# Kernel optimization log

Measured on AMD Instinct MI355X. Metric: run time of the kernel, lower is better.

## Reference

```python
import jax, jax.numpy as jnp
import numpy as np

OUT = 7            # output_size
SR = 2             # sampling_ratio (samples per bin per axis)
SCALES = (0.25, 0.125, 0.0625, 0.03125)
CANON_SIZE = 224.0
CANON_LVL = 4.0
MIN_LVL = 2
IMG = 800.0


def setup_inputs() -> dict:
    key = jax.random.key(0)
    kf = jax.random.split(key, 6)
    B, C, R = 2, 256, 256
    sizes = [200, 100, 50, 25]
    feats = [jax.random.normal(kf[i], (B, C, s, s), jnp.float32) for i, s in enumerate(sizes)]
    # valid xyxy boxes in [0, IMG], log-uniform side lengths -> spread across FPN levels
    ctr = jax.random.uniform(kf[4], (B, R, 2), minval=0.0, maxval=IMG)
    wh = jnp.exp(jax.random.uniform(kf[5], (B, R, 2), minval=float(np.log(16.0)), maxval=float(np.log(512.0))))
    lo = jnp.clip(ctr - wh / 2, 0.0, IMG)
    hi = jnp.clip(ctr + wh / 2, 0.0, IMG)
    boxes = jnp.concatenate([lo, hi], axis=-1)  # [B,R,4]
    return {"feat0": feats[0], "feat1": feats[1], "feat2": feats[2], "feat3": feats[3], "boxes": boxes}


def _prep(c, lim):
    """torchvision ROIAlign (aligned=False) bilinear index prep.
    c: sample coords [N,OUT,SR]; lim: per-box feature extent (H or W) [N]."""
    limb = lim[:, None, None]
    valid = (c > -1.0) & (c < limb)          # out-of-range samples contribute 0
    cc = jnp.maximum(c, 0.0)
    low = jnp.floor(cc)
    cap = limb - 1.0
    at_edge = low >= cap                      # y_low >= H-1 -> clamp, frac = 0
    low = jnp.minimum(low, cap)
    high = jnp.minimum(low + 1.0, cap)
    cc = jnp.where(at_edge, low, cc)
    frac = cc - low
    return valid, low.astype(jnp.int32), high.astype(jnp.int32), frac


def roi_pooler(feats, boxes):
    B, R = boxes.shape[0], boxes.shape[1]
    C = feats[0].shape[1]
    N = B * R
    flat = boxes.reshape(N, 4)
    bidx = jnp.repeat(jnp.arange(B, dtype=jnp.int32), R)  # batch index per ROI

    # level assignment (assign_boxes_to_levels)
    area = (flat[:, 2] - flat[:, 0]) * (flat[:, 3] - flat[:, 1])
    lvl = jnp.floor(CANON_LVL + jnp.log2(jnp.sqrt(area) / CANON_SIZE + 1e-8))
    lvl = jnp.clip(lvl, MIN_LVL, MIN_LVL + len(feats) - 1).astype(jnp.int32) - MIN_LVL  # [N] in [0,3]

    # pad all levels to P2 size and stack so each ROI is sampled once at its level
    Hm, Wm = feats[0].shape[2], feats[0].shape[3]
    padded = jnp.stack([jnp.pad(f, ((0, 0), (0, 0), (0, Hm - f.shape[2]), (0, Wm - f.shape[3]))) for f in feats])
    fp = padded.transpose(0, 1, 3, 4, 2)  # [L,B,Hm,Wm,C] channels-last for gather
    Hs = jnp.array([f.shape[2] for f in feats], jnp.float32)[lvl]
    Ws = jnp.array([f.shape[3] for f in feats], jnp.float32)[lvl]
    scale = jnp.array(SCALES, jnp.float32)[lvl]

    # ROIAlign aligned=False: scale coords, clamp roi size to >= 1
    x1 = flat[:, 0] * scale
    y1 = flat[:, 1] * scale
    x2 = flat[:, 2] * scale
    y2 = flat[:, 3] * scale
    roi_w = jnp.maximum(x2 - x1, 1.0)
    roi_h = jnp.maximum(y2 - y1, 1.0)
    bw = roi_w / OUT
    bh = roi_h / OUT

    # sample grid: bin index + sub-sample offsets -> [N,OUT,SR]
    grid = jnp.arange(OUT, dtype=jnp.float32)[None, :, None] + (jnp.arange(SR, dtype=jnp.float32)[None, None, :] + 0.5) / SR
    ys = y1[:, None, None] + bh[:, None, None] * grid
    xs = x1[:, None, None] + bw[:, None, None] * grid

    vy, yl, yh, fy = _prep(ys, Hs)
    vx, xl, xh, fx = _prep(xs, Ws)

    P = OUT * OUT * SR * SR  # all sample points per ROI

    def by(a):  # y-axis quantity -> broadcast over (out_y,out_x,sr_y,sr_x)
        return jnp.broadcast_to(a[:, :, None, :, None], (N, OUT, OUT, SR, SR)).reshape(N, P)

    def bx(a):
        return jnp.broadcast_to(a[:, None, :, None, :], (N, OUT, OUT, SR, SR)).reshape(N, P)

    YL, YH, FY, VY = by(yl), by(yh), by(fy), by(vy)
    XL, XH, FX, VX = bx(xl), bx(xh), bx(fx), bx(vx)

    li = lvl[:, None]
    bi = bidx[:, None]
    v00 = fp[li, bi, YL, XL]  # [N,P,C]
    v01 = fp[li, bi, YL, XH]
    v10 = fp[li, bi, YH, XL]
    v11 = fp[li, bi, YH, XH]

    w = lambda a: a[..., None]
    val = (w((1 - FY) * (1 - FX)) * v00 + w((1 - FY) * FX) * v01
           + w(FY * (1 - FX)) * v10 + w(FY * FX) * v11)
    val = val * w((VY & VX).astype(val.dtype))
    out = val.reshape(N, OUT, OUT, SR * SR, C).mean(axis=3)  # average over SR*SR samples
    return out.transpose(0, 3, 1, 2)  # [N,C,OUT,OUT]


def reference(feat0, feat1, feat2, feat3, boxes):
    return roi_pooler([feat0, feat1, feat2, feat3], boxes)
```

## Files before the change

kernel.cpp:

```cpp
#include <hip/hip_runtime.h>
#include <math.h>

typedef unsigned short u16;
typedef unsigned int   u32;

#define OUTSZ 7
#define B_ 2
#define C_ 256
#define R_ 256
#define N_ (B_ * R_)

#define PX_TOTAL 106250
#define WS_NEEDED ((size_t)PX_TOTAL * 256 * 2)

__device__ __forceinline__ u16 f2bf(float v) {
    u32 u = __float_as_uint(v);
    u += 0x7fffu + ((u >> 16) & 1u);
    return (u16)(u >> 16);
}

__device__ __forceinline__ u32 pack2bf(float a, float b) {
    return (u32)f2bf(a) | ((u32)f2bf(b) << 16);
}

__device__ __forceinline__ float bflo(u32 u) { return __uint_as_float(u << 16); }
__device__ __forceinline__ float bfhi(u32 u) { return __uint_as_float(u & 0xffff0000u); }

__global__ __launch_bounds__(512, 8) void nhwc_cast(
    const float* __restrict__ f0, const float* __restrict__ f1,
    const float* __restrict__ f2, const float* __restrict__ f3,
    u16* __restrict__ dst)
{
    __shared__ u32 lds32[256 * 32];
    const int tid  = threadIdx.x;
    const int lane = tid & 63;
    const int wave = tid >> 6;

    const int t  = blockIdx.x;
    const int cb = blockIdx.y;
    const int b  = blockIdx.z;
    const float* src; int HWsz, dstBase, ft;
    if      (t < 157) { src = f0; HWsz = 40000; dstBase = 0;      ft = t;       }
    else if (t < 197) { src = f1; HWsz = 10000; dstBase = 80000;  ft = t - 157; }
    else if (t < 207) { src = f2; HWsz = 2500;  dstBase = 100000; ft = t - 197; }
    else              { src = f3; HWsz = 625;   dstBase = 105000; ft = t - 207; }

    const int fbase = ft * 256;
    const int cw    = cb * 64 + wave * 8;
    const int rem   = HWsz - fbase;
    const int p0    = 4 * lane;
    const bool vec  = ((HWsz & 3) == 0) && (p0 + 3 < rem);

    const float* base = src + ((size_t)(b * C_ + cw)) * HWsz + fbase;

    float f[8][4];
    #pragma unroll
    for (int i = 0; i < 8; ++i) {
        const float* row = base + (size_t)i * HWsz;
        if (vec) {
            float4 v = *(const float4*)(row + p0);
            f[i][0] = v.x; f[i][1] = v.y; f[i][2] = v.z; f[i][3] = v.w;
        } else {
            #pragma unroll
            for (int k = 0; k < 4; ++k)
                f[i][k] = (p0 + k < rem) ? row[p0 + k] : 0.0f;
        }
    }

    #pragma unroll
    for (int j = 0; j < 4; ++j) {
        uint4 o;
        o.x = pack2bf(f[0][j], f[1][j]);
        o.y = pack2bf(f[2][j], f[3][j]);
        o.z = pack2bf(f[4][j], f[5][j]);
        o.w = pack2bf(f[6][j], f[7][j]);
        const int q = wave ^ (lane & 7);
        *(uint4*)&lds32[(p0 + j) * 32 + q * 4] = o;
    }
    __syncthreads();

    const int maxpx = rem < 256 ? rem : 256;
    #pragma unroll
    for (int i = 0; i < 4; ++i) {
        const int idx = i * 512 + tid;
        const int px  = idx >> 3;
        const int sub = idx & 7;
        if (px < maxpx) {
            const int q = sub ^ ((px >> 2) & 7);
            uint4 o = *(const uint4*)&lds32[px * 32 + q * 4];
            *(uint4*)(dst + (size_t)(dstBase + b * HWsz + fbase + px) * 256 + cb * 64 + sub * 8) = o;
        }
    }
}

__global__ __launch_bounds__(512) void roi_gather(
    const u16* __restrict__ ws16, const float* __restrict__ boxes,
    float* __restrict__ out)
{
    __shared__ float ldsO[49 * 264];
    __shared__ float s_wy0[14], s_wy1[14], s_wlo[14], s_whi[14];
    __shared__ int   s_yl[14], s_yh[14], s_xo[14];
    __shared__ int   s_base, s_W;

    const int n    = blockIdx.x;
    const int tid  = threadIdx.x;
    const int lane = tid & 63;
    const int wave = tid >> 6;

    if (tid < 28) {
        const float* bx = boxes + (size_t)n * 4;
        float x1 = bx[0], y1 = bx[1], x2 = bx[2], y2 = bx[3];
        float area = (x2 - x1) * (y2 - y1);
        float lf = floorf(4.0f + log2f(sqrtf(area) / 224.0f + 1e-8f));
        lf = fminf(fmaxf(lf, 2.0f), 5.0f);
        int lvl = (int)lf - 2;
        const float scales[4] = {0.25f, 0.125f, 0.0625f, 0.03125f};
        const int   sizes[4]  = {200, 100, 50, 25};
        const int   bases[4]  = {0, 80000, 100000, 105000};
        float scale = scales[lvl];
        int   HW    = sizes[lvl];
        float lim = (float)HW, cap = lim - 1.0f;
        float fx1 = x1 * scale, fy1 = y1 * scale;
        float bw = fmaxf(x2 * scale - fx1, 1.0f) / (float)OUTSZ;
        float bh = fmaxf(y2 * scale - fy1, 1.0f) / (float)OUTSZ;
        if (tid == 0) { s_base = bases[lvl] + (n >> 8) * HW * HW; s_W = HW; }

        const int  i   = (tid < 14) ? tid : tid - 14;
        const bool isy = tid < 14;
        float o  = isy ? fy1 : fx1;
        float st = isy ? bh  : bw;
        float gq = (float)(i >> 1) + ((float)(i & 1) + 0.5f) * 0.5f;
        float c = o + st * gq;
        bool  v = (c > -1.0f) && (c < lim);
        float cc = fmaxf(c, 0.0f);
        float low = floorf(cc);
        bool  edge = low >= cap;
        low = fminf(low, cap);
        float high = fminf(low + 1.0f, cap);
        float fr = edge ? 0.0f : (cc - low);
        float w0 = v ? (1.0f - fr) : 0.0f;
        float w1 = v ? fr : 0.0f;
        if (isy) {
            s_yl[i] = (int)low; s_yh[i] = (int)high; s_wy0[i] = w0; s_wy1[i] = w1;
        } else {
            int xl = (int)low, xh = (int)high;
            bool col = (xh == xl);
            s_xo[i]  = col ? xl - 1 : xl;
            s_wlo[i] = col ? 0.0f : w0;
            s_whi[i] = col ? (w0 + w1) : w1;
        }
    }
    __syncthreads();

    const int base = s_base, W = s_W;
    const bool hiHalf = lane >= 32;

    for (int cell = wave; cell < 49; cell += 8) {
        const int cu = __builtin_amdgcn_readfirstlane(cell);
        const int oy = cu / 7, ox = cu - oy * 7;
        float a0 = 0, a1 = 0, a2 = 0, a3 = 0, a4 = 0, a5 = 0, a6 = 0, a7 = 0;
        #pragma unroll
        for (int sy = 0; sy < 2; ++sy) {
            const int ei = oy * 2 + sy;
            const float wy0 = s_wy0[ei], wy1 = s_wy1[ei];
            const size_t rl = (size_t)(base + s_yl[ei] * W);
            const size_t rh = (size_t)(base + s_yh[ei] * W);
            #pragma unroll
            for (int sx = 0; sx < 2; ++sx) {
                const int ej = ox * 2 + sx;
                const int xo = s_xo[ej];
                const float wsel = hiHalf ? s_whi[ej] : s_wlo[ej];
                uint4 A = ((const uint4*)(ws16 + (rl + xo) * 256))[lane];
                const float wa = wy0 * wsel;
                a0 += wa * bflo(A.x); a1 += wa * bfhi(A.x);
                a2 += wa * bflo(A.y); a3 += wa * bfhi(A.y);
                a4 += wa * bflo(A.z); a5 += wa * bfhi(A.z);
                a6 += wa * bflo(A.w); a7 += wa * bfhi(A.w);
                uint4 Bv = ((const uint4*)(ws16 + (rh + xo) * 256))[lane];
                const float wb = wy1 * wsel;
                a0 += wb * bflo(Bv.x); a1 += wb * bfhi(Bv.x);
                a2 += wb * bflo(Bv.y); a3 += wb * bfhi(Bv.y);
                a4 += wb * bflo(Bv.z); a5 += wb * bfhi(Bv.z);
                a6 += wb * bflo(Bv.w); a7 += wb * bfhi(Bv.w);
            }
        }
        a0 += __shfl_xor(a0, 32); a1 += __shfl_xor(a1, 32);
        a2 += __shfl_xor(a2, 32); a3 += __shfl_xor(a3, 32);
        a4 += __shfl_xor(a4, 32); a5 += __shfl_xor(a5, 32);
        a6 += __shfl_xor(a6, 32); a7 += __shfl_xor(a7, 32);
        float* dstl = &ldsO[cu * 264 + (lane & 31) * 8 + (hiHalf ? 4 : 0)];
        float4 v = hiHalf ? make_float4(a4 * 0.25f, a5 * 0.25f, a6 * 0.25f, a7 * 0.25f)
                          : make_float4(a0 * 0.25f, a1 * 0.25f, a2 * 0.25f, a3 * 0.25f);
        *(float4*)dstl = v;
    }
    __syncthreads();

    float* op = out + (size_t)n * (C_ * 49);
    for (int i4 = tid; i4 < 3136; i4 += 512) {
        const int e = 4 * i4;
        float4 v;
        {   int c = e / 49,      r = e - 49 * c;          v.x = ldsO[r * 264 + c]; }
        {   int c = (e+1) / 49,  r = (e+1) - 49 * c;      v.y = ldsO[r * 264 + c]; }
        {   int c = (e+2) / 49,  r = (e+2) - 49 * c;      v.z = ldsO[r * 264 + c]; }
        {   int c = (e+3) / 49,  r = (e+3) - 49 * c;      v.w = ldsO[r * 264 + c]; }
        *(float4*)(op + e) = v;
    }
}

__global__ __launch_bounds__(256) void roi_direct(
    const float* __restrict__ f0, const float* __restrict__ f1,
    const float* __restrict__ f2, const float* __restrict__ f3,
    const float* __restrict__ boxes, float* __restrict__ out)
{
    const int total = B_ * R_ * C_ * OUTSZ * OUTSZ;
    int idx = blockIdx.x * blockDim.x + threadIdx.x;
    if (idx >= total) return;
    int ox = idx % 7, oy = (idx / 7) % 7, c = (idx / 49) % C_, n = idx / (49 * C_), b = n >> 8;
    const float* bx = boxes + (size_t)n * 4;
    float x1 = bx[0], y1 = bx[1], x2 = bx[2], y2 = bx[3];
    float lf = floorf(4.0f + log2f(sqrtf((x2 - x1) * (y2 - y1)) / 224.0f + 1e-8f));
    int lvl = (int)fminf(fmaxf(lf, 2.0f), 5.0f) - 2;
    const float scales[4] = {0.25f, 0.125f, 0.0625f, 0.03125f};
    const int sizes[4] = {200, 100, 50, 25};
    float scale = scales[lvl]; int HW = sizes[lvl];
    const float* fl = lvl == 0 ? f0 : lvl == 1 ? f1 : lvl == 2 ? f2 : f3;
    float fx1 = x1 * scale, fy1 = y1 * scale;
    float bw = fmaxf(x2 * scale - fx1, 1.0f) / 7.0f, bh = fmaxf(y2 * scale - fy1, 1.0f) / 7.0f;
    const float* plane = fl + ((size_t)(b * C_ + c)) * HW * HW;
    float lim = (float)HW, cap = lim - 1.0f, acc = 0.0f;
    #pragma unroll
    for (int sy = 0; sy < 2; sy++) {
        float yc = fy1 + bh * ((float)oy + ((float)sy + 0.5f) * 0.5f);
        bool vy = (yc > -1.0f) && (yc < lim);
        float ccy = fmaxf(yc, 0.0f), lowy = floorf(ccy);
        bool ey = lowy >= cap; lowy = fminf(lowy, cap);
        float highy = fminf(lowy + 1.0f, cap);
        float wfy = ey ? 0.0f : (ccy - lowy);
        int yl = (int)lowy, yh = (int)highy;
        #pragma unroll
        for (int sx = 0; sx < 2; sx++) {
            float xc = fx1 + bw * ((float)ox + ((float)sx + 0.5f) * 0.5f);
            bool vx = (xc > -1.0f) && (xc < lim);
            float ccx = fmaxf(xc, 0.0f), lowx = floorf(ccx);
            bool ex = lowx >= cap; lowx = fminf(lowx, cap);
            float highx = fminf(lowx + 1.0f, cap);
            float wfx = ex ? 0.0f : (ccx - lowx);
            int xl = (int)lowx, xh = (int)highx;
            if (vy && vx) {
                float v00 = plane[yl * HW + xl], v01 = plane[yl * HW + xh];
                float v10 = plane[yh * HW + xl], v11 = plane[yh * HW + xh];
                acc += (1.0f - wfy) * ((1.0f - wfx) * v00 + wfx * v01)
                     + wfy * ((1.0f - wfx) * v10 + wfx * v11);
            }
        }
    }
    out[idx] = acc * 0.25f;
}

extern "C" void kernel_launch(void* const* d_in, const int* in_sizes, int n_in,
                              void* d_out, int out_size, void* d_ws, size_t ws_size,
                              hipStream_t stream) {
    const float* f0    = (const float*)d_in[0];
    const float* f1    = (const float*)d_in[1];
    const float* f2    = (const float*)d_in[2];
    const float* f3    = (const float*)d_in[3];
    const float* boxes = (const float*)d_in[4];
    float* out = (float*)d_out;

    if (ws_size < WS_NEEDED) {
        const int total = B_ * R_ * C_ * OUTSZ * OUTSZ;
        roi_direct<<<(total + 255) / 256, 256, 0, stream>>>(f0, f1, f2, f3, boxes, out);
        return;
    }

    u16* nhwc = (u16*)d_ws;

    nhwc_cast<<<dim3(210, 4, 2), 512, 0, stream>>>(f0, f1, f2, f3, nhwc);
    roi_gather<<<dim3(N_), 512, 0, stream>>>(nhwc, boxes, out);
}
```

Before: 180.5 us.

## Split ROI gather across two channel-half blocks with two x-columns per wave

The gather kernel now launches two blocks per ROI, each handling 128 channels, which halves the per-block LDS staging buffer and doubles the block count. Within a wave, the two 32-lane halves now load adjacent x-columns (xo and xo+1) for 128 channels each, using 8-byte loads instead of 16-byte loads. A launch bound of 8 blocks per CU is added to raise occupancy. The cost is that each ROI's box and weight preparation is duplicated across both blocks, the loads are narrower, and only the lower half-wave writes results to LDS.

```diff
diff --git a/kernel.cpp b/kernel.cpp
--- a/kernel.cpp
+++ b/kernel.cpp
@@ -93,16 +93,17 @@
     }
 }
 
-__global__ __launch_bounds__(512) void roi_gather(
+__global__ __launch_bounds__(512, 8) void roi_gather(
     const u16* __restrict__ ws16, const float* __restrict__ boxes,
     float* __restrict__ out)
 {
-    __shared__ float ldsO[49 * 264];
+    __shared__ float ldsO[49 * 132];
     __shared__ float s_wy0[14], s_wy1[14], s_wlo[14], s_whi[14];
     __shared__ int   s_yl[14], s_yh[14], s_xo[14];
     __shared__ int   s_base, s_W;
 
-    const int n    = blockIdx.x;
+    const int g    = blockIdx.x;
+    const int n    = blockIdx.y;
     const int tid  = threadIdx.x;
     const int lane = tid & 63;
     const int wave = tid >> 6;
@@ -153,12 +154,15 @@
     __syncthreads();
 
     const int base = s_base, W = s_W;
+    const int co   = g * 64;
     const bool hiHalf = lane >= 32;
+    const int xsel = lane >> 5;
+    const int ck   = lane & 31;
 
     for (int cell = wave; cell < 49; cell += 8) {
         const int cu = __builtin_amdgcn_readfirstlane(cell);
         const int oy = cu / 7, ox = cu - oy * 7;
-        float a0 = 0, a1 = 0, a2 = 0, a3 = 0, a4 = 0, a5 = 0, a6 = 0, a7 = 0;
+        float a0 = 0, a1 = 0, a2 = 0, a3 = 0;
         #pragma unroll
         for (int sy = 0; sy < 2; ++sy) {
             const int ei = oy * 2 + sy;
@@ -170,40 +174,38 @@
                 const int ej = ox * 2 + sx;
                 const int xo = s_xo[ej];
                 const float wsel = hiHalf ? s_whi[ej] : s_wlo[ej];
-                uint4 A = ((const uint4*)(ws16 + (rl + xo) * 256))[lane];
+                uint2 A = ((const uint2*)((const u32*)(ws16 + (rl + xo + xsel) * 256) + co))[ck];
                 const float wa = wy0 * wsel;
                 a0 += wa * bflo(A.x); a1 += wa * bfhi(A.x);
                 a2 += wa * bflo(A.y); a3 += wa * bfhi(A.y);
-                a4 += wa * bflo(A.z); a5 += wa * bfhi(A.z);
-                a6 += wa * bflo(A.w); a7 += wa * bfhi(A.w);
-                uint4 Bv = ((const uint4*)(ws16 + (rh + xo) * 256))[lane];
+                uint2 Bv = ((const uint2*)((const u32*)(ws16 + (rh + xo + xsel) * 256) + co))[ck];
                 const float wb = wy1 * wsel;
                 a0 += wb * bflo(Bv.x); a1 += wb * bfhi(Bv.x);
                 a2 += wb * bflo(Bv.y); a3 += wb * bfhi(Bv.y);
-                a4 += wb * bflo(Bv.z); a5 += wb * bfhi(Bv.z);
-                a6 += wb * bflo(Bv.w); a7 += wb * bfhi(Bv.w);
             }
         }
         a0 += __shfl_xor(a0, 32); a1 += __shfl_xor(a1, 32);
         a2 += __shfl_xor(a2, 32); a3 += __shfl_xor(a3, 32);
-        a4 += __shfl_xor(a4, 32); a5 += __shfl_xor(a5, 32);
-        a6 += __shfl_xor(a6, 32); a7 += __shfl_xor(a7, 32);
-        float* dstl = &ldsO[cu * 264 + (lane & 31) * 8 + (hiHalf ? 4 : 0)];
-        float4 v = hiHalf ? make_float4(a4 * 0.25f, a5 * 0.25f, a6 * 0.25f, a7 * 0.25f)
-                          : make_float4(a0 * 0.25f, a1 * 0.25f, a2 * 0.25f, a3 * 0.25f);
-        *(float4*)dstl = v;
+        if (!hiHalf) {
+            float4 v = make_float4(a0 * 0.25f, a1 * 0.25f, a2 * 0.25f, a3 * 0.25f);
+            *(float4*)&ldsO[cu * 132 + ck * 4] = v;
+        }
     }
     __syncthreads();
 
-    float* op = out + (size_t)n * (C_ * 49);
-    for (int i4 = tid; i4 < 3136; i4 += 512) {
+    float* op = out + (size_t)n * (C_ * 49) + g * (128 * 49);
+    for (int i4 = tid; i4 < 1568; i4 += 512) {
         const int e = 4 * i4;
-        float4 v;
-        {   int c = e / 49,      r = e - 49 * c;          v.x = ldsO[r * 264 + c]; }
-        {   int c = (e+1) / 49,  r = (e+1) - 49 * c;      v.y = ldsO[r * 264 + c]; }
-        {   int c = (e+2) / 49,  r = (e+2) - 49 * c;      v.z = ldsO[r * 264 + c]; }
-        {   int c = (e+3) / 49,  r = (e+3) - 49 * c;      v.w = ldsO[r * 264 + c]; }
-        *(float4*)(op + e) = v;
+        int c0i = (e + 0) / 49, r0i = (e + 0) - 49 * c0i;
+        int c1i = (e + 1) / 49, r1i = (e + 1) - 49 * c1i;
+        int c2i = (e + 2) / 49, r2i = (e + 2) - 49 * c2i;
+        int c3i = (e + 3) / 49, r3i = (e + 3) - 49 * c3i;
+        float4 w;
+        w.x = ldsO[r0i * 132 + c0i];
+        w.y = ldsO[r1i * 132 + c1i];
+        w.z = ldsO[r2i * 132 + c2i];
+        w.w = ldsO[r3i * 132 + c3i];
+        *(float4*)(op + e) = w;
     }
 }
 
@@ -276,5 +278,5 @@
     u16* nhwc = (u16*)d_ws;
 
     nhwc_cast<<<dim3(210, 4, 2), 512, 0, stream>>>(f0, f1, f2, f3, nhwc);
-    roi_gather<<<dim3(N_), 512, 0, stream>>>(nhwc, boxes, out);
-}
+    roi_gather<<<dim3(2, N_), 512, 0, stream>>>(nhwc, boxes, out);
+}
```

After: 180.3 us. No clear change (-0.1%).
